# Performance work log

Measured on AMD Instinct MI355X. Metric: run time of the kernel, lower is better.

Reference implementation:

```python
import jax, jax.numpy as jnp
import numpy as np
import math

D_MODEL = 384
D_HEAD = 64
N_HEADS = D_MODEL // D_HEAD  # 6
COND = 768
KSIZE = 7
EPS = 1e-6


def setup_inputs() -> dict:
    key = jax.random.key(0)
    ks = jax.random.split(key, 8)
    n, h, w = 4, 128, 128
    x = jax.random.normal(ks[0], (n, h, w, D_MODEL), jnp.float32)
    pos = jax.random.uniform(ks[1], (n, h, w, 2), jnp.float32)
    cond = jax.random.normal(ks[2], (n, COND), jnp.float32)
    # AdaRMSNorm linear (zero-init in original; small random so it exercises the math)
    w_cond = jax.random.normal(ks[3], (COND, D_MODEL), jnp.float32) * 0.02
    w_qkv = jax.random.normal(ks[4], (D_MODEL, 3 * D_MODEL), jnp.float32) * (D_MODEL ** -0.5)
    scale = jnp.full((N_HEADS,), 10.0, jnp.float32)
    # AxialRoPE freqs: exp(linspace(log(pi), log(10pi), n_heads*dim//4+1)[:-1]).view(dim//4, nh).T
    dim = D_HEAD // 2
    freqs = jnp.exp(jnp.linspace(math.log(math.pi), math.log(10.0 * math.pi),
                                 N_HEADS * (dim // 4) + 1)[:-1])
    freqs = freqs.reshape(dim // 4, N_HEADS).T  # [n_heads, d_head//8]
    w_out = jax.random.normal(ks[5], (D_MODEL, D_MODEL), jnp.float32) * 0.02
    return {"x": x, "pos": pos, "cond": cond, "w_cond": w_cond, "w_qkv": w_qkv,
            "scale": scale, "freqs": freqs, "w_out": w_out}


def rms_norm(x, scale):
    return x * jax.lax.rsqrt(jnp.mean(x * x, axis=-1, keepdims=True) + EPS) * scale


def apply_rotary(x, theta):
    # rotate the first 2*d channels of the head dim, leave the rest untouched
    d = theta.shape[-1]
    x1, x2, x3 = x[..., :d], x[..., d:2 * d], x[..., 2 * d:]
    c, s = jnp.cos(theta), jnp.sin(theta)
    return jnp.concatenate([x1 * c - x2 * s, x2 * c + x1 * s, x3], axis=-1)


def nb_idx(L):
    # NATTEN clamped neighborhood: window start = clip(i - k//2, 0, L-k)
    start = jnp.clip(jnp.arange(L) - KSIZE // 2, 0, L - KSIZE)
    return start[None, :] + jnp.arange(KSIZE)[:, None]  # [KSIZE, L]


def reference(x, pos, cond, w_cond, w_qkv, scale, freqs, w_out):
    n, H, W, _ = x.shape
    skip = x
    # AdaRMSNorm
    x = rms_norm(x, (cond @ w_cond)[:, None, None, :] + 1.0)
    # QKV projection, 'n h w (t nh e) -> t n nh h w e'
    qkv = (x @ w_qkv).reshape(n, H, W, 3, N_HEADS, D_HEAD)
    qkv = jnp.transpose(qkv, (3, 0, 4, 1, 2, 5))
    q, k, v = qkv[0], qkv[1], qkv[2]  # [n, nh, H, W, e]
    # cosine-sim scaling with learned per-head scale
    sq = jnp.sqrt(scale)[:, None, None, None]
    q = q * (sq * jax.lax.rsqrt(jnp.sum(q * q, axis=-1, keepdims=True) + EPS))
    k = k * (sq * jax.lax.rsqrt(jnp.sum(k * k, axis=-1, keepdims=True) + EPS))
    # axial RoPE: theta [n,H,W,nh,d_head//4] per axis -> cat -> movedim(-2,-4)
    th = pos[..., None, 0:1] * freqs
    tw = pos[..., None, 1:2] * freqs
    theta = jnp.moveaxis(jnp.concatenate([th, tw], axis=-1), -2, -4)  # [n,nh,H,W,dd]
    q = apply_rotary(q, theta)
    k = apply_rotary(k, theta)
    # neighborhood attention (na2d_qk / softmax / na2d_av), dilation 1
    ih_all = nb_idx(H)  # [k, H]
    iw_all = nb_idx(W)  # [k, W]
    hh = jnp.repeat(jnp.arange(KSIZE), KSIZE)
    ww = jnp.tile(jnp.arange(KSIZE), KSIZE)
    idx_h = ih_all[hh]  # [k*k, H]
    idx_w = iw_all[ww]  # [k*k, W]

    def qk_step(_, hw):
        ih, iw = hw
        ks_ = k[:, :, ih, :, :][:, :, :, iw, :]  # keys at this window offset
        return None, jnp.einsum('nchwe,nchwe->nchw', q, ks_)

    _, qk = jax.lax.scan(qk_step, None, (idx_h, idx_w))  # [k*k, n, nh, H, W]
    a = jax.nn.softmax(qk, axis=0)  # softmax over the k*k window

    def av_step(acc, inp):
        (ih, iw), at = inp
        vs = v[:, :, ih, :, :][:, :, :, iw, :]
        return acc + at[..., None] * vs, None

    out, _ = jax.lax.scan(av_step, jnp.zeros_like(v), ((idx_h, idx_w), a))
    # 'n nh h w e -> n h w (nh e)'
    out = jnp.transpose(out, (0, 2, 3, 1, 4)).reshape(n, H, W, N_HEADS * D_HEAD)
    return out @ w_out + skip
```

## Files before the change

kernel.cpp:

```cpp
#include <hip/hip_runtime.h>
#include <hip/hip_bf16.h>

#define DM 384
#define NH 6
#define DH 64
#define CD 768
#define NBATCH 4
#define IMH 128
#define IMW 128
#define HEADPIX (IMH*IMW)
#define NPIX (NBATCH*IMH*IMW)
#define PLANE ((size_t)NPIX*DM)
#define KS 7
#define EPSF 1e-6f

typedef __attribute__((ext_vector_type(8))) short bf16x8v;
typedef __attribute__((ext_vector_type(4))) short bf16x4v;
typedef __attribute__((ext_vector_type(4))) float f32x4v;
typedef __attribute__((ext_vector_type(4))) unsigned short u16x4;

#define GLOAD_LDS16(g, l) __builtin_amdgcn_global_load_lds( \
    (const __attribute__((address_space(1))) void*)(g), \
    (__attribute__((address_space(3))) void*)(l), 16, 0, 0)

#define TR64(dst, p, imm) asm volatile("ds_read_b64_tr_b16 %0, %1 offset:" #imm \
    : "=v"(dst) : "v"((const __attribute__((address_space(3))) char*)(p)))

__device__ __forceinline__ unsigned short f2bf(float f){
    __hip_bfloat16 h = __float2bfloat16(f);
    return *reinterpret_cast<unsigned short*>(&h);
}
__device__ __forceinline__ bf16x8v cat8(bf16x4v lo, bf16x4v hi){
    bf16x8v r;
    r[0]=lo[0]; r[1]=lo[1]; r[2]=lo[2]; r[3]=lo[3];
    r[4]=hi[0]; r[5]=hi[1]; r[6]=hi[2]; r[7]=hi[3];
    return r;
}

__device__ __forceinline__ bf16x8v frag8(const __hip_bfloat16* base, int row, int kelem){
    int byteoff = row*128 + ((kelem*2) ^ ((row & 7) << 4));
    return *(const bf16x8v*)((const char*)base + byteoff);
}
__device__ __forceinline__ bf16x8v frag512(const char* base, int row, int kelem){
    int byteoff = row*512 + ((kelem*2) ^ ((row & 7) << 4));
    return *(const bf16x8v*)(base + byteoff);
}

__global__ __launch_bounds__(256) void k_cond(const float* __restrict__ cond,
                                              const float* __restrict__ wc,
                                              float* __restrict__ sc){
    __shared__ float red[4][64];
    const int b = blockIdx.x;
    const int n = b / 6, j0 = (b - n*6) * 64;
    const int lane = threadIdx.x & 63, wave = threadIdx.x >> 6;
    const float* cr = cond + n*CD + wave*192;
    const float* wp = wc + (size_t)(wave*192)*DM + j0 + lane;
    float acc = 0.f;
    #pragma unroll 4
    for (int i = 0; i < 192; ++i) acc += cr[i] * wp[(size_t)i*DM];
    red[wave][lane] = acc;
    __syncthreads();
    if (threadIdx.x < 64) {
        float s = red[0][lane] + red[1][lane] + red[2][lane] + red[3][lane];
        sc[n*DM + j0 + lane] = s + 1.0f;
    }
}

__global__ __launch_bounds__(256) void k_xscale(const float* __restrict__ x,
                                                const float* __restrict__ sc,
                                                __hip_bfloat16* __restrict__ xb){
    int row  = blockIdx.x*4 + (threadIdx.x>>6);
    int lane = threadIdx.x & 63;
    int n    = row >> 14;
    const float* xr  = x + (size_t)row*DM;
    const float* scp = sc + n*DM;
    float v[6];
    float s = 0.f;
    #pragma unroll
    for (int i=0;i<6;++i){ v[i] = xr[i*64+lane]; s += v[i]*v[i]; }
    #pragma unroll
    for (int o=32;o;o>>=1) s += __shfl_xor(s,o);
    float r = rsqrtf(s*(1.0f/DM) + EPSF);
    #pragma unroll
    for (int i=0;i<6;++i)
        xb[(size_t)row*DM + i*64+lane] = __float2bfloat16(v[i]*r*scp[i*64+lane]);
}

__global__ void k_cvtwq(const float* __restrict__ wq, __hip_bfloat16* __restrict__ wqb){
    int id = blockIdx.x*256 + threadIdx.x;
    if (id >= 3*DM*DM) return;
    int nn = id / DM, kk = id - nn*DM;
    wqb[id] = __float2bfloat16(wq[(size_t)kk*(3*DM) + nn]);
}
__global__ void k_cvtwo(const float* __restrict__ wo, __hip_bfloat16* __restrict__ wob){
    int id = blockIdx.x*256 + threadIdx.x;
    if (id >= DM*DM) return;
    int nn = id / DM, kk = id - nn*DM;
    wob[id] = __float2bfloat16(wo[(size_t)kk*DM + nn]);
}

__global__ __launch_bounds__(256) void k_qkv_mfma(
    const __hip_bfloat16* __restrict__ xb, const __hip_bfloat16* __restrict__ wqb,
    const float* __restrict__ pos, const float* __restrict__ freqs,
    const float* __restrict__ scale, __hip_bfloat16* __restrict__ qkv)
{
    __shared__ char As[2*16384];
    __shared__ char Bs[2*16384];
    const int t    = threadIdx.x;
    const int lane = t & 63;
    const int wave = t >> 6;
    const int swzb = (blockIdx.x & 7)*576 + (blockIdx.x >> 3);
    const int jb = swzb % 9;
    const int mb = swzb / 9;
    const int j0 = jb*128, m0 = mb*128;
    const int n  = m0 >> 14;
    const int wr = (wave >> 1) * 64;
    const int wc = (wave & 1) * 64;
    const int fr = lane & 15;
    const int fg = lane >> 4;

    f32x4v acc[4][4] = {};

#define STAGE_QKV(buf, k0) \
    { _Pragma("unroll") \
      for (int i = 0; i < 4; ++i) { \
        int off = (i*256 + t) * 8; \
        int row = off >> 6; \
        int col = (off & 63) ^ ((row & 7) << 3); \
        GLOAD_LDS16(xb  + (size_t)(m0 + row)*DM + (k0) + col, \
                    As + (buf)*16384 + (i*256 + (wave<<6))*16); \
        GLOAD_LDS16(wqb + (size_t)(j0 + row)*DM + (k0) + col, \
                    Bs + (buf)*16384 + (i*256 + (wave<<6))*16); \
      } }

    STAGE_QKV(0, 0)
    #pragma unroll
    for (int kt = 0; kt < 6; ++kt) {
        const int cur = kt & 1;
        if (kt < 5) {
            STAGE_QKV(cur ^ 1, (kt+1)*64)
            asm volatile("s_waitcnt vmcnt(8)" ::: "memory");
        } else {
            asm volatile("s_waitcnt vmcnt(0)" ::: "memory");
        }
        asm volatile("s_barrier" ::: "memory");
        const __hip_bfloat16* Ab = (const __hip_bfloat16*)(As + cur*16384);
        const __hip_bfloat16* Bb = (const __hip_bfloat16*)(Bs + cur*16384);
        #pragma unroll
        for (int kk = 0; kk < 64; kk += 32) {
            bf16x8v af[4], bfr[4];
            #pragma unroll
            for (int i = 0; i < 4; ++i) af[i]  = frag8(Ab, wr + i*16 + fr, kk + fg*8);
            #pragma unroll
            for (int i = 0; i < 4; ++i) bfr[i] = frag8(Bb, wc + i*16 + fr, kk + fg*8);
            #pragma unroll
            for (int i = 0; i < 4; ++i)
            #pragma unroll
            for (int j = 0; j < 4; ++j)
                acc[i][j] = __builtin_amdgcn_mfma_f32_16x16x32_bf16(bfr[i], af[j], acc[i][j], 0, 0, 0);
        }
        asm volatile("s_barrier" ::: "memory");
    }
#undef STAGE_QKV

    const int t_ = jb / 3;
    const int pj = jb - t_*3;
    const int c  = pj*2 + (wc >> 6);
    const size_t hbase = (size_t)t_*PLANE + (((size_t)(n*NH + c)*HEADPIX) << 6);

    if (t_ < 2) {
        const float sq = sqrtf(scale[c]);
        const float4 f4 = *(const float4*)(freqs + c*8 + ((fg & 1) << 2));
        float fqv[4] = {f4.x, f4.y, f4.z, f4.w};
        #pragma unroll
        for (int ni = 0; ni < 4; ++ni) {
            int m = m0 + wr + ni*16 + fr;
            float ss = 0.f;
            #pragma unroll
            for (int i = 0; i < 4; ++i)
                #pragma unroll
                for (int r = 0; r < 4; ++r) ss += acc[i][ni][r]*acc[i][ni][r];
            ss += __shfl_xor(ss, 16);
            ss += __shfl_xor(ss, 32);
            float rn = sq * rsqrtf(ss + EPSF);
            float2 pp = *(const float2*)(pos + (size_t)m*2);
            float pc = (fg < 2) ? pp.x : pp.y;
            u16x4 o0, o1, o2, o3;
            #pragma unroll
            for (int r = 0; r < 4; ++r) {
                float th = pc * fqv[r];
                float ct = __cosf(th), st = __sinf(th);
                float a0 = acc[0][ni][r]*rn, a1 = acc[1][ni][r]*rn;
                o0[r] = f2bf(a0*ct - a1*st);
                o1[r] = f2bf(a1*ct + a0*st);
                o2[r] = f2bf(acc[2][ni][r]*rn);
                o3[r] = f2bf(acc[3][ni][r]*rn);
            }
            size_t base = hbase + ((size_t)(m & (HEADPIX-1)) << 6) + (fg << 2);
            *(u16x4*)(qkv + base     ) = o0;
            *(u16x4*)(qkv + base + 16) = o1;
            *(u16x4*)(qkv + base + 32) = o2;
            *(u16x4*)(qkv + base + 48) = o3;
        }
    } else {
        #pragma unroll
        for (int ni = 0; ni < 4; ++ni) {
            int m = m0 + wr + ni*16 + fr;
            size_t base = hbase + ((size_t)(m & (HEADPIX-1)) << 6) + (fg << 2);
            #pragma unroll
            for (int i = 0; i < 4; ++i) {
                u16x4 pk;
                #pragma unroll
                for (int r = 0; r < 4; ++r) pk[r] = f2bf(acc[i][ni][r]);
                *(u16x4*)(qkv + base + i*16) = pk;
            }
        }
    }
}

__global__ __launch_bounds__(256) void k_attn2(
    const __hip_bfloat16* __restrict__ q, const __hip_bfloat16* __restrict__ kbuf,
    const __hip_bfloat16* __restrict__ vbuf, __hip_bfloat16* __restrict__ attn)
{
    __shared__ char smem[61440];
    char* KP = smem;
    char* VT = smem + 32768;

    const int t    = threadIdx.x;
    const int lane = t & 63;
    const int wave = t >> 6;
    const int fr   = lane & 15;
    const int fg   = lane >> 4;

    const int tile = blockIdx.x;
    const int n6c  = blockIdx.y;
    const int h0 = (tile >> 4) << 3;
    const int w0 = (tile & 15) << 3;
    const int nn = n6c / NH;
    const int cc = n6c - nn*NH;

    const size_t pixbase = (size_t)n6c << 14;
    const __hip_bfloat16* qp = q    + (pixbase << 6);
    const __hip_bfloat16* kp = kbuf + (pixbase << 6);
    const __hip_bfloat16* vp = vbuf + (pixbase << 6);

    const int u0h = min(max(h0-3,0), IMH-7);
    const int u0w = min(max(w0-3,0), IMW-7);

    const int q_l = (wave<<4) + fr;
    const int qh = h0 + (q_l >> 3), qw = w0 + (q_l & 7);
    const __hip_bfloat16* qrow = qp + (((size_t)qh*IMW + qw) << 6);
    bf16x8v aq0 = *(const bf16x8v*)(qrow + fg*8);
    bf16x8v aq1 = *(const bf16x8v*)(qrow + 32 + fg*8);
    __builtin_amdgcn_sched_barrier(0);

    #pragma unroll
    for (int it = 0; it < 7; ++it) {
        int chunk = it*256 + t;
        int key  = chunk >> 3;
        int part = chunk & 7;
        int kh = min(u0h + (key >> 4), IMH-1);
        int kw = min(u0w + (key & 15), IMW-1);
        GLOAD_LDS16(kp + (((size_t)kh*IMW + kw) << 6) + ((part ^ (key & 7)) << 3),
                    KP + (it*256 + (wave<<6))*16);
    }
    #pragma unroll
    for (int it = 0; it < 7; ++it) {
        int chunk = it*256 + t;
        int keyq = chunk >> 5;
        int rem  = chunk & 31;
        int key  = (keyq << 2) + ((rem >> 1) & 3);
        int d0   = ((rem >> 3) << 4) + ((chunk & 1) << 3);
        int kh = min(u0h + (key >> 4), IMH-1);
        int kw = min(u0w + (key & 15), IMW-1);
        GLOAD_LDS16(vp + (((size_t)kh*IMW + kw) << 6) + d0,
                    VT + (it*256 + (wave<<6))*16);
    }

    int loh[4], low_[4];
    #pragma unroll
    for (int r = 0; r < 4; ++r) {
        int qr  = (wave<<4) + fg*4 + r;
        int qhr = h0 + (qr >> 3), qwr = w0 + (qr & 7);
        loh[r]  = min(max(qhr-3,0), IMH-7) - u0h;
        low_[r] = min(max(qwr-3,0), IMW-7) - u0w;
    }

    asm volatile("s_waitcnt vmcnt(7)" ::: "memory");
    asm volatile("s_barrier" ::: "memory");

    f32x4v acc_s[14];
    #pragma unroll
    for (int nf = 0; nf < 14; ++nf) {
        bf16x8v b0 = frag8((const __hip_bfloat16*)KP, nf*16 + fr, fg*8);
        bf16x8v b1 = frag8((const __hip_bfloat16*)KP, nf*16 + fr, 32 + fg*8);
        f32x4v s = {0.f,0.f,0.f,0.f};
        s = __builtin_amdgcn_mfma_f32_16x16x32_bf16(aq0, b0, s, 0, 0, 0);
        s = __builtin_amdgcn_mfma_f32_16x16x32_bf16(aq1, b1, s, 0, 0, 0);
        acc_s[nf] = s;
    }

    float rs[4] = {0.f,0.f,0.f,0.f};
    #pragma unroll
    for (int nf = 0; nf < 14; ++nf) {
        int key = nf*16 + fr;
        int uh = key >> 4;
        int uw = key & 15;
        #pragma unroll
        for (int r = 0; r < 4; ++r) {
            bool ok = ((unsigned)(uh - loh[r]) <= 6u) && ((unsigned)(uw - low_[r]) <= 6u);
            float pv = ok ? __expf(acc_s[nf][r]) : 0.f;
            acc_s[nf][r] = pv;
            rs[r] += pv;
        }
    }
    #pragma unroll
    for (int o = 1; o < 16; o <<= 1) {
        #pragma unroll
        for (int r = 0; r < 4; ++r) rs[r] += __shfl_xor(rs[r], o);
    }
    float rinv[4];
    #pragma unroll
    for (int r = 0; r < 4; ++r) rinv[r] = 1.0f / rs[r];

    asm volatile("s_barrier" ::: "memory");

    #pragma unroll
    for (int nf = 0; nf < 14; ++nf) {
        int key = nf*16 + fr;
        #pragma unroll
        for (int r = 0; r < 4; ++r) {
            int qr = (wave<<4) + fg*4 + r;
            *(__hip_bfloat16*)(KP + qr*512 + ((key*2) ^ ((qr & 7) << 4))) = __float2bfloat16(acc_s[nf][r]);
        }
    }
    asm volatile("s_waitcnt vmcnt(0) lgkmcnt(0)" ::: "memory");
    asm volatile("s_barrier" ::: "memory");
    __builtin_amdgcn_sched_barrier(0);

    f32x4v acc_o[4] = {};
    const char* vlane = VT + ((lane >> 4) << 10) + ((lane & 15) << 3);
    #pragma unroll
    for (int kst = 0; kst < 7; ++kst) {
        bf16x8v a = frag512(KP, (wave<<4) + fr, kst*32 + fg*8);
        const char* vk = vlane + kst*4096;
        bf16x4v t0a, t0b, t1a, t1b, t2a, t2b, t3a, t3b;
        TR64(t0a, vk,   0); TR64(t0b, vk, 512);
        TR64(t1a, vk, 128); TR64(t1b, vk, 640);
        TR64(t2a, vk, 256); TR64(t2b, vk, 768);
        TR64(t3a, vk, 384); TR64(t3b, vk, 896);
        asm volatile("s_waitcnt lgkmcnt(0)" ::: "memory");
        __builtin_amdgcn_sched_barrier(0);
        acc_o[0] = __builtin_amdgcn_mfma_f32_16x16x32_bf16(a, cat8(t0a,t0b), acc_o[0], 0, 0, 0);
        acc_o[1] = __builtin_amdgcn_mfma_f32_16x16x32_bf16(a, cat8(t1a,t1b), acc_o[1], 0, 0, 0);
        acc_o[2] = __builtin_amdgcn_mfma_f32_16x16x32_bf16(a, cat8(t2a,t2b), acc_o[2], 0, 0, 0);
        acc_o[3] = __builtin_amdgcn_mfma_f32_16x16x32_bf16(a, cat8(t3a,t3b), acc_o[3], 0, 0, 0);
    }

    #pragma unroll
    for (int nf = 0; nf < 4; ++nf) {
        int d = cc*64 + nf*16 + fr;
        #pragma unroll
        for (int r = 0; r < 4; ++r) {
            int qr  = (wave<<4) + fg*4 + r;
            int qhr = h0 + (qr >> 3), qwr = w0 + (qr & 7);
            size_t pix = ((size_t)nn << 14) + (size_t)qhr*IMW + qwr;
            attn[pix*DM + d] = __float2bfloat16(acc_o[nf][r] * rinv[r]);
        }
    }
}

__global__ __launch_bounds__(256) void k_out_mfma(
    const __hip_bfloat16* __restrict__ attn, const __hip_bfloat16* __restrict__ wob,
    const float* __restrict__ xin, float* __restrict__ out)
{
    __shared__ char As[2*16384];
    __shared__ char Bs[2*16384];
    const int t    = threadIdx.x;
    const int lane = t & 63;
    const int wave = t >> 6;
    const int swzb = (blockIdx.x & 7)*192 + (blockIdx.x >> 3);
    const int jb = swzb % 3;
    const int mb = swzb / 3;
    const int j0 = jb*128, m0 = mb*128;
    const int wr = (wave >> 1) * 64;
    const int wc = (wave & 1) * 64;
    const int fr = lane & 15;
    const int fg = lane >> 4;

    f32x4v acc[4][4] = {};

#define STAGE_OUT(buf, k0) \
    { _Pragma("unroll") \
      for (int i = 0; i < 4; ++i) { \
        int off = (i*256 + t) * 8; \
        int row = off >> 6; \
        int col = (off & 63) ^ ((row & 7) << 3); \
        GLOAD_LDS16(attn + (size_t)(m0 + row)*DM + (k0) + col, \
                    As + (buf)*16384 + (i*256 + (wave<<6))*16); \
        GLOAD_LDS16(wob  + (size_t)(j0 + row)*DM + (k0) + col, \
                    Bs + (buf)*16384 + (i*256 + (wave<<6))*16); \
      } }

    STAGE_OUT(0, 0)
    #pragma unroll
    for (int kt = 0; kt < 6; ++kt) {
        const int cur = kt & 1;
        if (kt < 5) {
            STAGE_OUT(cur ^ 1, (kt+1)*64)
            asm volatile("s_waitcnt vmcnt(8)" ::: "memory");
        } else {
            asm volatile("s_waitcnt vmcnt(0)" ::: "memory");
        }
        asm volatile("s_barrier" ::: "memory");
        const __hip_bfloat16* Ab = (const __hip_bfloat16*)(As + cur*16384);
        const __hip_bfloat16* Bb = (const __hip_bfloat16*)(Bs + cur*16384);
        #pragma unroll
        for (int kk = 0; kk < 64; kk += 32) {
            bf16x8v af[4], bfr[4];
            #pragma unroll
            for (int i = 0; i < 4; ++i) af[i]  = frag8(Ab, wr + i*16 + fr, kk + fg*8);
            #pragma unroll
            for (int i = 0; i < 4; ++i) bfr[i] = frag8(Bb, wc + i*16 + fr, kk + fg*8);
            #pragma unroll
            for (int i = 0; i < 4; ++i)
            #pragma unroll
            for (int j = 0; j < 4; ++j)
                acc[i][j] = __builtin_amdgcn_mfma_f32_16x16x32_bf16(bfr[i], af[j], acc[i][j], 0, 0, 0);
        }
        asm volatile("s_barrier" ::: "memory");
    }
#undef STAGE_OUT

    #pragma unroll
    for (int i = 0; i < 4; ++i) {
        int jg = j0 + wc + i*16 + (fg<<2);
        #pragma unroll
        for (int ni = 0; ni < 4; ++ni) {
            int m = m0 + wr + ni*16 + fr;
            size_t idx = (size_t)m*DM + jg;
            float4 xv = *(const float4*)(xin + idx);
            float4 ov;
            ov.x = acc[i][ni][0] + xv.x;
            ov.y = acc[i][ni][1] + xv.y;
            ov.z = acc[i][ni][2] + xv.z;
            ov.w = acc[i][ni][3] + xv.w;
            *(float4*)(out + idx) = ov;
        }
    }
}

extern "C" void kernel_launch(void* const* d_in, const int* in_sizes, int n_in,
                              void* d_out, int out_size, void* d_ws, size_t ws_size,
                              hipStream_t stream) {
    const float* x      = (const float*)d_in[0];
    const float* pos    = (const float*)d_in[1];
    const float* cond   = (const float*)d_in[2];
    const float* w_cond = (const float*)d_in[3];
    const float* w_qkv  = (const float*)d_in[4];
    const float* scale  = (const float*)d_in[5];
    const float* freqs  = (const float*)d_in[6];
    const float* w_out  = (const float*)d_in[7];
    float* out = (float*)d_out;

    char* ws = (char*)d_ws;
    __hip_bfloat16* xb   = (__hip_bfloat16*)ws;
    __hip_bfloat16* attn = (__hip_bfloat16*)ws;
    __hip_bfloat16* qkv  = (__hip_bfloat16*)(ws + 50331648);
    float* s_cond = (float*)(ws + 201326592);
    __hip_bfloat16* wqb = (__hip_bfloat16*)(ws + 201332736);
    __hip_bfloat16* qb = qkv;
    __hip_bfloat16* kb = qkv + PLANE;
    __hip_bfloat16* vb = qkv + 2*PLANE;
    __hip_bfloat16* wob = qkv;

    k_cvtwq<<<1728, 256, 0, stream>>>(w_qkv, wqb);
    k_cond<<<24, 256, 0, stream>>>(cond, w_cond, s_cond);
    k_xscale<<<NPIX/4, 256, 0, stream>>>(x, s_cond, xb);
    k_qkv_mfma<<<4608, 256, 0, stream>>>(xb, wqb, pos, freqs, scale, qkv);
    k_attn2<<<dim3(256, 24), 256, 0, stream>>>(qb, kb, vb, attn);
    k_cvtwo<<<576, 256, 0, stream>>>(w_out, wob);
    k_out_mfma<<<1536, 256, 0, stream>>>(attn, wob, x, out);
}
```

Measured before the change: 277.3 us.

## Load QKV GEMM MFMA fragments directly from global memory instead of LDS

Removes the double-buffered LDS staging (global_load_lds with swizzle, waitcnt and barriers) in the QKV projection GEMM. Each wave now reads its A and B MFMA fragments straight from global memory with 16-byte vector loads. This drops the LDS footprint and the barriers, which may raise occupancy, but loses cross-wave sharing of tiles. Each tile row is now fetched by two waves through cache, and latency is no longer hidden by explicit prefetch.

```diff
diff --git a/kernel.cpp b/kernel.cpp
--- a/kernel.cpp
+++ b/kernel.cpp
@@ -104,8 +104,6 @@
     const float* __restrict__ pos, const float* __restrict__ freqs,
     const float* __restrict__ scale, __hip_bfloat16* __restrict__ qkv)
 {
-    __shared__ char As[2*16384];
-    __shared__ char Bs[2*16384];
     const int t    = threadIdx.x;
     const int lane = t & 63;
     const int wave = t >> 6;
@@ -121,47 +119,31 @@
 
     f32x4v acc[4][4] = {};
 
-#define STAGE_QKV(buf, k0) \
-    { _Pragma("unroll") \
-      for (int i = 0; i < 4; ++i) { \
-        int off = (i*256 + t) * 8; \
-        int row = off >> 6; \
-        int col = (off & 63) ^ ((row & 7) << 3); \
-        GLOAD_LDS16(xb  + (size_t)(m0 + row)*DM + (k0) + col, \
-                    As + (buf)*16384 + (i*256 + (wave<<6))*16); \
-        GLOAD_LDS16(wqb + (size_t)(j0 + row)*DM + (k0) + col, \
-                    Bs + (buf)*16384 + (i*256 + (wave<<6))*16); \
-      } }
-
-    STAGE_QKV(0, 0)
+    const __hip_bfloat16* ap[4];
+    const __hip_bfloat16* bp[4];
+    #pragma unroll
+    for (int i = 0; i < 4; ++i) {
+        ap[i] = xb  + (size_t)(m0 + wr + i*16 + fr)*DM + fg*8;
+        bp[i] = wqb + (size_t)(j0 + wc + i*16 + fr)*DM + fg*8;
+    }
+
     #pragma unroll
     for (int kt = 0; kt < 6; ++kt) {
-        const int cur = kt & 1;
-        if (kt < 5) {
-            STAGE_QKV(cur ^ 1, (kt+1)*64)
-            asm volatile("s_waitcnt vmcnt(8)" ::: "memory");
-        } else {
-            asm volatile("s_waitcnt vmcnt(0)" ::: "memory");
-        }
-        asm volatile("s_barrier" ::: "memory");
-        const __hip_bfloat16* Ab = (const __hip_bfloat16*)(As + cur*16384);
-        const __hip_bfloat16* Bb = (const __hip_bfloat16*)(Bs + cur*16384);
-        #pragma unroll
-        for (int kk = 0; kk < 64; kk += 32) {
+        #pragma unroll
+        for (int kk = 0; kk < 2; ++kk) {
+            const int ke = kt*64 + kk*32;
             bf16x8v af[4], bfr[4];
             #pragma unroll
-            for (int i = 0; i < 4; ++i) af[i]  = frag8(Ab, wr + i*16 + fr, kk + fg*8);
-            #pragma unroll
-            for (int i = 0; i < 4; ++i) bfr[i] = frag8(Bb, wc + i*16 + fr, kk + fg*8);
+            for (int i = 0; i < 4; ++i) af[i]  = *(const bf16x8v*)(ap[i] + ke);
+            #pragma unroll
+            for (int i = 0; i < 4; ++i) bfr[i] = *(const bf16x8v*)(bp[i] + ke);
             #pragma unroll
             for (int i = 0; i < 4; ++i)
             #pragma unroll
             for (int j = 0; j < 4; ++j)
                 acc[i][j] = __builtin_amdgcn_mfma_f32_16x16x32_bf16(bfr[i], af[j], acc[i][j], 0, 0, 0);
         }
-        asm volatile("s_barrier" ::: "memory");
-    }
-#undef STAGE_QKV
+    }
 
     const int t_ = jb / 3;
     const int pj = jb - t_*3;
```

Measured after the change: 400.6 us. 44.5% more time.
